# Kernel optimization log

Hardware: AMD Instinct MI355X
Metric: run time of the kernel (lower is better)

The kernel has to match this reference:

```python
import jax, jax.numpy as jnp
import numpy as np
from jax import lax

WIN = 9
PAD = WIN // 2
WIN3 = WIN ** 3


def _box_sum(x):
    """Separable 3D box-filter local sum. x: [N, 1, D, H, W].
    Mathematically identical to conv3d with a ones([1,1,WIN,WIN,WIN]) kernel,
    padding=PAD, but done as three 1D passes (O(3*WIN) instead of O(WIN^3))."""
    dn = ('NCDHW', 'OIDHW', 'NCDHW')
    for axis in range(3):  # D, H, W
        kshape = [1, 1, 1, 1, 1]
        kshape[2 + axis] = WIN
        kern = jnp.ones(kshape, dtype=x.dtype)
        padding = [(0, 0), (0, 0), (0, 0)]
        padding[axis] = (PAD, PAD)
        x = lax.conv_general_dilated(x, kern, window_strides=(1, 1, 1),
                                     padding=padding, dimension_numbers=dn)
    return x


def setup_inputs() -> dict:
    key = jax.random.key(0)
    k1, k2 = jax.random.split(key)
    shape = (2, 1, 160, 192, 160)
    predicted = jax.random.normal(k1, shape, dtype=jnp.float32)
    target = jax.random.normal(k2, shape, dtype=jnp.float32)
    return {"predicted": predicted, "target": target}


def reference(predicted, target):
    I = predicted
    J = target
    # Batch the 5 independent box-sums in one conv call by folding into batch.
    stacked = jnp.concatenate([I, J, I * I, J * J, I * J], axis=0)  # [5B,1,D,H,W]
    sums = _box_sum(stacked)
    I_sum, J_sum, I2_sum, J2_sum, IJ_sum = jnp.split(sums, 5, axis=0)

    u_I = I_sum / WIN3
    u_J = J_sum / WIN3

    cross = IJ_sum - u_J * I_sum - u_I * J_sum + u_I * u_J * WIN3
    I_var = I2_sum - 2.0 * u_I * I_sum + u_I * u_I * WIN3
    J_var = J2_sum - 2.0 * u_J * J_sum + u_J * u_J * WIN3

    cc = cross * cross / (I_var * J_var + 1e-05)
    return jnp.mean(cc)
```

## Files before the change

### kernel.cpp

```cpp
#include <hip/hip_runtime.h>

#define Bv   2
#define Dd   160
#define Hh   192
#define Ww   160
#define HW   (Hh*Ww)
#define DHW  (Dd*Hh*Ww)
#define NTOT (Bv*DHW)
#define INV729 (1.0f/729.0f)

typedef _Float16 f16;

__device__ __forceinline__ float4 LD4(const float* p) {
    return *reinterpret_cast<const float4*>(p);
}
__device__ __forceinline__ float4 LD4(const f16* p) {
    union { uint2 u; f16 h[4]; } c;
    c.u = *reinterpret_cast<const uint2*>(p);
    return make_float4((float)c.h[0], (float)c.h[1], (float)c.h[2], (float)c.h[3]);
}
__device__ __forceinline__ void ST4(float* p, float4 v) {
    *reinterpret_cast<float4*>(p) = v;
}
__device__ __forceinline__ void ST4(f16* p, float4 v) {
    union { uint2 u; f16 h[4]; } c;
    c.h[0] = (f16)v.x; c.h[1] = (f16)v.y; c.h[2] = (f16)v.z; c.h[3] = (f16)v.w;
    *reinterpret_cast<uint2*>(p) = c.u;
}
__device__ __forceinline__ float4 add4(float4 a, float4 b) {
    return make_float4(a.x+b.x, a.y+b.y, a.z+b.z, a.w+b.w);
}
__device__ __forceinline__ float4 sub4(float4 a, float4 b) {
    return make_float4(a.x-b.x, a.y-b.y, a.z-b.z, a.w-b.w);
}
__device__ __forceinline__ float4 mul4(float4 a, float4 b) {
    return make_float4(a.x*b.x, a.y*b.y, a.z*b.z, a.w*b.w);
}
__device__ __forceinline__ float4 zero4() { return make_float4(0.f,0.f,0.f,0.f); }

__device__ __forceinline__ void rowsum5(const float* __restrict__ rI,
                                        const float* __restrict__ rJ,
                                        int x0, float sgn, float4 S[5]) {
    float4 vI[3], vJ[3];
    if (x0 >= 4 && x0 <= Ww - 8) {
        vI[0] = LD4(rI + x0 - 4); vI[1] = LD4(rI + x0); vI[2] = LD4(rI + x0 + 4);
        vJ[0] = LD4(rJ + x0 - 4); vJ[1] = LD4(rJ + x0); vJ[2] = LD4(rJ + x0 + 4);
    } else {
        float wI[12], wJ[12];
        #pragma unroll
        for (int i = 0; i < 12; ++i) {
            int xx = x0 - 4 + i;
            bool ok = (xx >= 0) && (xx < Ww);
            wI[i] = ok ? rI[xx] : 0.f;
            wJ[i] = ok ? rJ[xx] : 0.f;
        }
        vI[0] = make_float4(wI[0],wI[1],wI[2],wI[3]);
        vI[1] = make_float4(wI[4],wI[5],wI[6],wI[7]);
        vI[2] = make_float4(wI[8],wI[9],wI[10],wI[11]);
        vJ[0] = make_float4(wJ[0],wJ[1],wJ[2],wJ[3]);
        vJ[1] = make_float4(wJ[4],wJ[5],wJ[6],wJ[7]);
        vJ[2] = make_float4(wJ[8],wJ[9],wJ[10],wJ[11]);
    }
#define CH(cidx, E0, E1, E2) {                                              \
        float4 t0 = (E0), t1 = (E1), t2 = (E2);                             \
        float4 w = add4(t0, t1);                                            \
        float s0 = ((w.x + w.y) + (w.z + w.w)) + t2.x;                      \
        float s1 = s0 - t0.x + t2.y;                                        \
        float s2 = s1 - t0.y + t2.z;                                        \
        float s3 = s2 - t0.z + t2.w;                                        \
        S[cidx].x += sgn * s0; S[cidx].y += sgn * s1;                       \
        S[cidx].z += sgn * s2; S[cidx].w += sgn * s3;                       \
    }
    CH(0, vI[0], vI[1], vI[2]);
    CH(1, vJ[0], vJ[1], vJ[2]);
    CH(2, mul4(vI[0],vI[0]), mul4(vI[1],vI[1]), mul4(vI[2],vI[2]));
    CH(3, mul4(vJ[0],vJ[0]), mul4(vJ[1],vJ[1]), mul4(vJ[2],vJ[2]));
    CH(4, mul4(vI[0],vJ[0]), mul4(vI[1],vJ[1]), mul4(vI[2],vJ[2]));
#undef CH
}

__device__ __forceinline__ float cc4(const float4 S[5]) {
    float acc = 0.f;
#define FIN(CMP) {                                                      \
        float SI = S[0].CMP, SJ = S[1].CMP, SII = S[2].CMP,             \
              SJJ = S[3].CMP, SIJ = S[4].CMP;                           \
        float uI = SI * INV729, uJ = SJ * INV729;                       \
        float cross = SIJ - uJ * SI - uI * SJ + uI * uJ * 729.0f;       \
        float Iv = SII - 2.0f * uI * SI + uI * uI * 729.0f;             \
        float Jv = SJJ - 2.0f * uJ * SJ + uJ * uJ * 729.0f;             \
        acc += cross * cross / (Iv * Jv + 1e-5f);                       \
    }
    FIN(x) FIN(y) FIN(z) FIN(w)
#undef FIN
    return acc;
}

__device__ __forceinline__ void block_reduce_atomic(float acc, float* out) {
    for (int off = 32; off > 0; off >>= 1) acc += __shfl_down(acc, off);
    __shared__ float red[4];
    int lane = threadIdx.x & 63, wid = threadIdx.x >> 6;
    if (lane == 0) red[wid] = acc;
    __syncthreads();
    if (threadIdx.x == 0)
        atomicAdd(out, (red[0]+red[1]+red[2]+red[3]) * (1.0f/(float)NTOT));
}

template<typename TS>
__global__ __launch_bounds__(256)
void k12_xy(const float* __restrict__ I, const float* __restrict__ J,
            TS* __restrict__ B) {
    int tid = blockIdx.x * 256 + threadIdx.x;
    int x4 = tid % (Ww/4);  int t1 = tid / (Ww/4);
    int yc = t1 % (Hh/16);  t1 /= (Hh/16);
    int z  = t1 % Dd;       int b = t1 / Dd;
    int x0 = x4 * 4, y0 = yc * 16;

    const float* sI = I + (size_t)b * DHW + (size_t)z * HW;
    const float* sJ = J + (size_t)b * DHW + (size_t)z * HW;
    TS* dst = B + (size_t)b * DHW + (size_t)z * HW + x0;

    float4 S[5] = {zero4(), zero4(), zero4(), zero4(), zero4()};
    #pragma unroll
    for (int dy = -4; dy <= 3; ++dy) {
        int y = y0 + dy;
        if (y >= 0) rowsum5(sI + (size_t)y * Ww, sJ + (size_t)y * Ww, x0, 1.f, S);
    }
    #pragma unroll 4
    for (int y = y0; y < y0 + 16; ++y) {
        int yt = y + 4;
        if (yt < Hh) rowsum5(sI + (size_t)yt * Ww, sJ + (size_t)yt * Ww, x0, 1.f, S);
        ST4(dst + (size_t)y * Ww,                    S[0]);
        ST4(dst + (size_t)NTOT     + (size_t)y * Ww, S[1]);
        ST4(dst + (size_t)2 * NTOT + (size_t)y * Ww, S[2]);
        ST4(dst + (size_t)3 * NTOT + (size_t)y * Ww, S[3]);
        ST4(dst + (size_t)4 * NTOT + (size_t)y * Ww, S[4]);
        int yo = y - 4;
        if (yo >= 0) rowsum5(sI + (size_t)yo * Ww, sJ + (size_t)yo * Ww, x0, -1.f, S);
    }
}

template<typename TS>
__global__ __launch_bounds__(256)
void k3_zpass(const TS* __restrict__ Bb, float* __restrict__ out) {
    int tid = blockIdx.x * 256 + threadIdx.x;
    int x4 = tid % (Ww/4);  int t1 = tid / (Ww/4);
    int y  = t1 % Hh;       t1 /= Hh;
    int zc = t1 % (Dd/8);   int b = t1 / (Dd/8);
    int z0 = zc * 8;

    size_t base = (size_t)b * DHW + (size_t)y * Ww + x4 * 4;
    const TS* P0 = Bb + base;

    float4 S[5] = {zero4(), zero4(), zero4(), zero4(), zero4()};

#define LOADADD(zi) {                                                   \
        const TS* pp = P0 + (size_t)(zi) * HW;                          \
        S[0] = add4(S[0], LD4(pp));                                     \
        S[1] = add4(S[1], LD4(pp + (size_t)NTOT));                      \
        S[2] = add4(S[2], LD4(pp + (size_t)2 * NTOT));                  \
        S[3] = add4(S[3], LD4(pp + (size_t)3 * NTOT));                  \
        S[4] = add4(S[4], LD4(pp + (size_t)4 * NTOT));                  \
    }
#define LOADSUB(zi) {                                                   \
        const TS* pp = P0 + (size_t)(zi) * HW;                          \
        S[0] = sub4(S[0], LD4(pp));                                     \
        S[1] = sub4(S[1], LD4(pp + (size_t)NTOT));                      \
        S[2] = sub4(S[2], LD4(pp + (size_t)2 * NTOT));                  \
        S[3] = sub4(S[3], LD4(pp + (size_t)3 * NTOT));                  \
        S[4] = sub4(S[4], LD4(pp + (size_t)4 * NTOT));                  \
    }

    #pragma unroll
    for (int dz = -4; dz <= 3; ++dz) {
        int z = z0 + dz;
        if (z >= 0) LOADADD(z);
    }

    float acc = 0.f;
    #pragma unroll
    for (int z = z0; z < z0 + 8; ++z) {
        int zt = z + 4;
        if (zt < Dd) LOADADD(zt);
        acc += cc4(S);
        int zo = z - 4;
        if (zo >= 0) LOADSUB(zo);
    }
#undef LOADADD
#undef LOADSUB

    block_reduce_atomic(acc, out);
}

__global__ __launch_bounds__(256)
void k_brute(const float* __restrict__ I, const float* __restrict__ J,
             float* __restrict__ out) {
    int tid = blockIdx.x * 256 + threadIdx.x;
    int x4 = tid % (Ww/4);  int t1 = tid / (Ww/4);
    int y  = t1 % Hh;       t1 /= Hh;
    int z  = t1 % Dd;       int b = t1 / Dd;
    int x0 = x4 * 4;

    const float* bI = I + (size_t)b * DHW;
    const float* bJ = J + (size_t)b * DHW;

    float4 S[5] = {zero4(), zero4(), zero4(), zero4(), zero4()};
    for (int dz = -4; dz <= 4; ++dz) {
        int zz = z + dz;
        if (zz < 0 || zz >= Dd) continue;
        for (int dy = -4; dy <= 4; ++dy) {
            int yy = y + dy;
            if (yy < 0 || yy >= Hh) continue;
            rowsum5(bI + (size_t)zz * HW + (size_t)yy * Ww,
                    bJ + (size_t)zz * HW + (size_t)yy * Ww, x0, 1.f, S);
        }
    }
    block_reduce_atomic(cc4(S), out);
}

extern "C" void kernel_launch(void* const* d_in, const int* in_sizes, int n_in,
                              void* d_out, int out_size, void* d_ws, size_t ws_size,
                              hipStream_t stream) {
    const float* I = (const float*)d_in[0];
    const float* J = (const float*)d_in[1];
    float* out = (float*)d_out;

    hipMemsetAsync(d_out, 0, sizeof(float), stream);

    const int g12 = 153600/256;
    const int g3  = 307200/256;

    if (ws_size >= (size_t)5 * NTOT * sizeof(f16)) {
        f16* B = (f16*)d_ws;
        k12_xy<f16><<<g12, 256, 0, stream>>>(I, J, B);
        k3_zpass<f16><<<g3, 256, 0, stream>>>(B, out);
    } else {
        k_brute<<<(NTOT/4)/256, 256, 0, stream>>>(I, J, out);
    }
}
```

Before: 239.0 us.

## Software-pipeline row and slice loads with branchless weights in both passes

Both the xy pass and the z pass now prefetch the entering and leaving rows/slices two and one steps ahead, in register double buffers. Out-of-range indices are clamped, and the conditional add/subtract becomes an FMA with a 0/±1 weight, so the loops are fully unrolled and free of branches. Launch bounds gain min-blocks hints (2 and 4). The aim is to hide global-load latency behind the sliding-window arithmetic, at the cost of more registers and some redundant clamped loads at the boundaries.

```diff
diff --git a/kernel.cpp b/kernel.cpp
--- a/kernel.cpp
+++ b/kernel.cpp
@@ -30,18 +30,17 @@
 __device__ __forceinline__ float4 add4(float4 a, float4 b) {
     return make_float4(a.x+b.x, a.y+b.y, a.z+b.z, a.w+b.w);
 }
-__device__ __forceinline__ float4 sub4(float4 a, float4 b) {
-    return make_float4(a.x-b.x, a.y-b.y, a.z-b.z, a.w-b.w);
-}
 __device__ __forceinline__ float4 mul4(float4 a, float4 b) {
     return make_float4(a.x*b.x, a.y*b.y, a.z*b.z, a.w*b.w);
 }
+__device__ __forceinline__ float4 fma4(float4 s, float w, float4 v) {
+    return make_float4(fmaf(w,v.x,s.x), fmaf(w,v.y,s.y), fmaf(w,v.z,s.z), fmaf(w,v.w,s.w));
+}
 __device__ __forceinline__ float4 zero4() { return make_float4(0.f,0.f,0.f,0.f); }
 
-__device__ __forceinline__ void rowsum5(const float* __restrict__ rI,
+__device__ __forceinline__ void loadrow(const float* __restrict__ rI,
                                         const float* __restrict__ rJ,
-                                        int x0, float sgn, float4 S[5]) {
-    float4 vI[3], vJ[3];
+                                        int x0, float4 vI[3], float4 vJ[3]) {
     if (x0 >= 4 && x0 <= Ww - 8) {
         vI[0] = LD4(rI + x0 - 4); vI[1] = LD4(rI + x0); vI[2] = LD4(rI + x0 + 4);
         vJ[0] = LD4(rJ + x0 - 4); vJ[1] = LD4(rJ + x0); vJ[2] = LD4(rJ + x0 + 4);
@@ -61,6 +60,10 @@
         vJ[1] = make_float4(wJ[4],wJ[5],wJ[6],wJ[7]);
         vJ[2] = make_float4(wJ[8],wJ[9],wJ[10],wJ[11]);
     }
+}
+
+__device__ __forceinline__ void accum5(const float4 vI[3], const float4 vJ[3],
+                                       float sgn, float4 S[5]) {
 #define CH(cidx, E0, E1, E2) {                                              \
         float4 t0 = (E0), t1 = (E1), t2 = (E2);                             \
         float4 w = add4(t0, t1);                                            \
@@ -68,8 +71,7 @@
         float s1 = s0 - t0.x + t2.y;                                        \
         float s2 = s1 - t0.y + t2.z;                                        \
         float s3 = s2 - t0.z + t2.w;                                        \
-        S[cidx].x += sgn * s0; S[cidx].y += sgn * s1;                       \
-        S[cidx].z += sgn * s2; S[cidx].w += sgn * s3;                       \
+        S[cidx] = fma4(S[cidx], sgn, make_float4(s0, s1, s2, s3));          \
     }
     CH(0, vI[0], vI[1], vI[2]);
     CH(1, vJ[0], vJ[1], vJ[2]);
@@ -106,7 +108,7 @@
 }
 
 template<typename TS>
-__global__ __launch_bounds__(256)
+__global__ __launch_bounds__(256, 2)
 void k12_xy(const float* __restrict__ I, const float* __restrict__ J,
             TS* __restrict__ B) {
     int tid = blockIdx.x * 256 + threadIdx.x;
@@ -120,27 +122,64 @@
     TS* dst = B + (size_t)b * DHW + (size_t)z * HW + x0;
 
     float4 S[5] = {zero4(), zero4(), zero4(), zero4(), zero4()};
+
     #pragma unroll
     for (int dy = -4; dy <= 3; ++dy) {
         int y = y0 + dy;
-        if (y >= 0) rowsum5(sI + (size_t)y * Ww, sJ + (size_t)y * Ww, x0, 1.f, S);
-    }
-    #pragma unroll 4
-    for (int y = y0; y < y0 + 16; ++y) {
-        int yt = y + 4;
-        if (yt < Hh) rowsum5(sI + (size_t)yt * Ww, sJ + (size_t)yt * Ww, x0, 1.f, S);
+        if (y >= 0) {
+            float4 vI[3], vJ[3];
+            loadrow(sI + (size_t)y * Ww, sJ + (size_t)y * Ww, x0, vI, vJ);
+            accum5(vI, vJ, 1.f, S);
+        }
+    }
+
+    float4 aI[2][3], aJ[2][3], bI[2][3], bJ[2][3];
+    #pragma unroll
+    for (int k = 0; k < 2; ++k) {
+        int yt = y0 + 4 + k; if (yt > Hh - 1) yt = Hh - 1;
+        int yo = y0 - 4 + k; if (yo < 0) yo = 0;
+        loadrow(sI + (size_t)yt * Ww, sJ + (size_t)yt * Ww, x0, aI[k], aJ[k]);
+        loadrow(sI + (size_t)yo * Ww, sJ + (size_t)yo * Ww, x0, bI[k], bJ[k]);
+    }
+
+    #pragma unroll
+    for (int k = 0; k < 16; ++k) {
+        int y = y0 + k;
+        float4 nI[3], nJ[3], mI[3], mJ[3];
+        if (k < 14) {
+            int yt = y + 6; if (yt > Hh - 1) yt = Hh - 1;
+            int yo = y - 2; if (yo < 0) yo = 0;
+            loadrow(sI + (size_t)yt * Ww, sJ + (size_t)yt * Ww, x0, nI, nJ);
+            loadrow(sI + (size_t)yo * Ww, sJ + (size_t)yo * Ww, x0, mI, mJ);
+        }
+        float wA = (y + 4) < Hh ? 1.f : 0.f;
+        float wS = (y - 4) >= 0 ? -1.f : 0.f;
+
+        accum5(aI[0], aJ[0], wA, S);
         ST4(dst + (size_t)y * Ww,                    S[0]);
         ST4(dst + (size_t)NTOT     + (size_t)y * Ww, S[1]);
         ST4(dst + (size_t)2 * NTOT + (size_t)y * Ww, S[2]);
         ST4(dst + (size_t)3 * NTOT + (size_t)y * Ww, S[3]);
         ST4(dst + (size_t)4 * NTOT + (size_t)y * Ww, S[4]);
-        int yo = y - 4;
-        if (yo >= 0) rowsum5(sI + (size_t)yo * Ww, sJ + (size_t)yo * Ww, x0, -1.f, S);
+        accum5(bI[0], bJ[0], wS, S);
+
+        #pragma unroll
+        for (int j = 0; j < 3; ++j) {
+            aI[0][j] = aI[1][j]; aJ[0][j] = aJ[1][j];
+            bI[0][j] = bI[1][j]; bJ[0][j] = bJ[1][j];
+        }
+        if (k < 14) {
+            #pragma unroll
+            for (int j = 0; j < 3; ++j) {
+                aI[1][j] = nI[j]; aJ[1][j] = nJ[j];
+                bI[1][j] = mI[j]; bJ[1][j] = mJ[j];
+            }
+        }
     }
 }
 
 template<typename TS>
-__global__ __launch_bounds__(256)
+__global__ __launch_bounds__(256, 4)
 void k3_zpass(const TS* __restrict__ Bb, float* __restrict__ out) {
     int tid = blockIdx.x * 256 + threadIdx.x;
     int x4 = tid % (Ww/4);  int t1 = tid / (Ww/4);
@@ -153,40 +192,57 @@
 
     float4 S[5] = {zero4(), zero4(), zero4(), zero4(), zero4()};
 
-#define LOADADD(zi) {                                                   \
-        const TS* pp = P0 + (size_t)(zi) * HW;                          \
-        S[0] = add4(S[0], LD4(pp));                                     \
-        S[1] = add4(S[1], LD4(pp + (size_t)NTOT));                      \
-        S[2] = add4(S[2], LD4(pp + (size_t)2 * NTOT));                  \
-        S[3] = add4(S[3], LD4(pp + (size_t)3 * NTOT));                  \
-        S[4] = add4(S[4], LD4(pp + (size_t)4 * NTOT));                  \
-    }
-#define LOADSUB(zi) {                                                   \
-        const TS* pp = P0 + (size_t)(zi) * HW;                          \
-        S[0] = sub4(S[0], LD4(pp));                                     \
-        S[1] = sub4(S[1], LD4(pp + (size_t)NTOT));                      \
-        S[2] = sub4(S[2], LD4(pp + (size_t)2 * NTOT));                  \
-        S[3] = sub4(S[3], LD4(pp + (size_t)3 * NTOT));                  \
-        S[4] = sub4(S[4], LD4(pp + (size_t)4 * NTOT));                  \
-    }
-
     #pragma unroll
     for (int dz = -4; dz <= 3; ++dz) {
         int z = z0 + dz;
-        if (z >= 0) LOADADD(z);
+        if (z >= 0) {
+            const TS* pp = P0 + (size_t)z * HW;
+            #pragma unroll
+            for (int c = 0; c < 5; ++c) S[c] = add4(S[c], LD4(pp + (size_t)c * NTOT));
+        }
+    }
+
+    float4 A[5], Bf[5];
+    {
+        int zt = z0 + 4; if (zt > Dd - 1) zt = Dd - 1;
+        int zo = z0 - 4; if (zo < 0) zo = 0;
+        const TS* pa = P0 + (size_t)zt * HW;
+        const TS* pb = P0 + (size_t)zo * HW;
+        #pragma unroll
+        for (int c = 0; c < 5; ++c) {
+            A[c]  = LD4(pa + (size_t)c * NTOT);
+            Bf[c] = LD4(pb + (size_t)c * NTOT);
+        }
     }
 
     float acc = 0.f;
     #pragma unroll
-    for (int z = z0; z < z0 + 8; ++z) {
-        int zt = z + 4;
-        if (zt < Dd) LOADADD(zt);
+    for (int k = 0; k < 8; ++k) {
+        int z = z0 + k;
+        float4 nA[5], nB[5];
+        if (k < 7) {
+            int zt = z + 5; if (zt > Dd - 1) zt = Dd - 1;
+            int zo = z - 3; if (zo < 0) zo = 0;
+            const TS* pa = P0 + (size_t)zt * HW;
+            const TS* pb = P0 + (size_t)zo * HW;
+            #pragma unroll
+            for (int c = 0; c < 5; ++c) {
+                nA[c] = LD4(pa + (size_t)c * NTOT);
+                nB[c] = LD4(pb + (size_t)c * NTOT);
+            }
+        }
+        float wA = (z + 4) < Dd  ? 1.f  : 0.f;
+        float wS = (z - 4) >= 0 ? -1.f : 0.f;
+        #pragma unroll
+        for (int c = 0; c < 5; ++c) S[c] = fma4(S[c], wA, A[c]);
         acc += cc4(S);
-        int zo = z - 4;
-        if (zo >= 0) LOADSUB(zo);
-    }
-#undef LOADADD
-#undef LOADSUB
+        #pragma unroll
+        for (int c = 0; c < 5; ++c) S[c] = fma4(S[c], wS, Bf[c]);
+        if (k < 7) {
+            #pragma unroll
+            for (int c = 0; c < 5; ++c) { A[c] = nA[c]; Bf[c] = nB[c]; }
+        }
+    }
 
     block_reduce_atomic(acc, out);
 }
@@ -210,8 +266,10 @@
         for (int dy = -4; dy <= 4; ++dy) {
             int yy = y + dy;
             if (yy < 0 || yy >= Hh) continue;
-            rowsum5(bI + (size_t)zz * HW + (size_t)yy * Ww,
-                    bJ + (size_t)zz * HW + (size_t)yy * Ww, x0, 1.f, S);
+            float4 vI[3], vJ[3];
+            loadrow(bI + (size_t)zz * HW + (size_t)yy * Ww,
+                    bJ + (size_t)zz * HW + (size_t)yy * Ww, x0, vI, vJ);
+            accum5(vI, vJ, 1.f, S);
         }
     }
     block_reduce_atomic(cc4(S), out);
```

After: 699.2 us. 193% more time.
